# Kernel tuning notes

Hardware: AMD Instinct MI355X
Metric: run time of the kernel (lower is better)

## Reference

```python
import jax, jax.numpy as jnp
import numpy as np

IN_DIM, OUT_DIM = 128, 128
NUM, K = 5, 3            # knot intervals, spline order
SIZE = IN_DIM * OUT_DIM
BATCH = 512
NOISE = 0.1


def extend_knots_uniform(grid, k):
    # grid: (s, n_knots). Uniformly extend by k knots on each side.
    if k <= 0:
        return grid
    step = (grid[:, -1:] - grid[:, :1]) / (grid.shape[1] - 1)  # (s,1)
    left = grid[:, :1] - step * jnp.arange(k, 0, -1, dtype=grid.dtype)[None, :]
    right = grid[:, -1:] + step * jnp.arange(1, k + 1, dtype=grid.dtype)[None, :]
    return jnp.concatenate([left, grid, right], axis=1)


def cox_deboor(x, t, k):
    # x: (s, n), t: (s, m) extended knots -> B: (s, m-1-k, n)
    xt = x[:, None, :]                                   # (s,1,n)
    B = ((xt >= t[:, :-1, None]) & (xt < t[:, 1:, None])).astype(x.dtype)  # (s, m-1, n)
    m = t.shape[1]
    for r in range(1, k + 1):
        denom_a = jnp.maximum(t[:, r:m - 1] - t[:, :m - 1 - r], 1e-14)
        alpha = (xt - t[:, :m - 1 - r, None]) / denom_a[:, :, None]
        denom_b = jnp.maximum(t[:, r + 1:m] - t[:, 1:m - r], 1e-14)
        beta = (t[:, r + 1:m, None] - xt) / denom_b[:, :, None]
        B = alpha * B[:, :-1, :] + beta * B[:, 1:, :]    # (s, m-1-r, n)
    return B


def setup_inputs() -> dict:
    key = jax.random.key(0)
    kx, kc = jax.random.split(key)
    x = jax.random.normal(kx, (BATCH, IN_DIM), dtype=jnp.float32)
    knots = jnp.linspace(-1.0, 1.0, NUM + 1, dtype=jnp.float32)
    grid = jnp.tile(knots[None, :], (SIZE, 1))                       # (size, num+1)
    coef = jax.random.normal(kc, (SIZE, NUM + K), dtype=jnp.float32) * NOISE
    scale_base = jnp.ones((SIZE,), dtype=jnp.float32)
    scale_sp = jnp.ones((SIZE,), dtype=jnp.float32)
    mask = jnp.ones((SIZE,), dtype=jnp.float32)
    return {"x": x, "grid": grid, "coef": coef,
            "scale_base": scale_base, "scale_sp": scale_sp, "mask": mask}


def reference(x, grid, coef, scale_base, scale_sp, mask):
    batch = x.shape[0]
    # einsum('ij,k->ikj').reshape(b, size).T : row o*in_dim+i holds x[:, i]
    x_exp = jnp.tile(x, (1, OUT_DIM)).T                  # (size, batch)
    base_act = jax.nn.silu(x_exp)
    t_ext = extend_knots_uniform(grid, K)                # (size, num+1+2k)
    B = cox_deboor(x_exp, t_ext, K)                      # (size, num+k, batch)
    spline_val = jnp.einsum('sbn,sb->sn', B, coef)       # (size, batch)
    out = (scale_base[:, None] * base_act + scale_sp[:, None] * spline_val) * mask[:, None]
    out3 = out.reshape(OUT_DIM, IN_DIM, batch)           # permute(2,0,1).sum(dim=2)
    return out3.sum(axis=1).T                            # (batch, out_dim)
```

## Files before the change

kernel.cpp:

```cpp
#include <hip/hip_runtime.h>
#include <math.h>

constexpr int IN_DIM  = 128;
constexpr int OUT_DIM = 128;
constexpr int BATCH   = 512;
constexpr int NQ      = 8;
constexpr int TN = 8;
constexpr int TO = 32;
constexpr int NSEG = 8;
constexpr int SEGI = IN_DIM / NSEG;

__global__ __launch_bounds__(256, 1) void kan_kernel(
    const float* __restrict__ x,
    const float* __restrict__ grid,
    const float* __restrict__ coef,
    const float* __restrict__ scale_base,
    const float* __restrict__ scale_sp,
    const float* __restrict__ mask,
    float* __restrict__ out)
{
    __shared__ float Ps[TN][IN_DIM * NQ];
    __shared__ float Pb[TN][IN_DIM];
    __shared__ float red[NSEG][TN][TO];

    const int t  = threadIdx.x;
    const int n0 = (blockIdx.x >> 2) * TN;
    const int o0 = (blockIdx.x & 3) * TO;

    const float g0 = grid[0];
    const float g5 = grid[5];
    const float h  = (g5 - g0) * 0.2f;
    float tk[12];
    tk[0] = g0 - 3.f * h; tk[1] = g0 - 2.f * h; tk[2] = g0 - h;
    tk[3] = grid[0]; tk[4] = grid[1]; tk[5] = grid[2];
    tk[6] = grid[3]; tk[7] = grid[4]; tk[8] = grid[5];
    tk[9] = g5 + h; tk[10] = g5 + 2.f * h; tk[11] = g5 + 3.f * h;

    #pragma unroll
    for (int rep = 0; rep < 4; rep++) {
        const int p  = t + rep * 256;
        const int nl = p >> 7;
        const int i  = p & 127;
        const float xv = x[(n0 + nl) * IN_DIM + i];

        Pb[nl][i] = xv / (1.0f + __expf(-xv));

        float B[11];
        #pragma unroll
        for (int j = 0; j < 11; j++)
            B[j] = (xv >= tk[j] && xv < tk[j + 1]) ? 1.0f : 0.0f;
        #pragma unroll
        for (int r = 1; r <= 3; r++) {
            #pragma unroll
            for (int j = 0; j + r < 11; j++) {
                const float da = fmaxf(tk[j + r] - tk[j],     1e-14f);
                const float db = fmaxf(tk[j + r + 1] - tk[j + 1], 1e-14f);
                B[j] = (xv - tk[j]) / da * B[j] + (tk[j + r + 1] - xv) / db * B[j + 1];
            }
        }
        #pragma unroll
        for (int j = 0; j < NQ; j++) Ps[nl][i * NQ + j] = B[j];
    }
    __syncthreads();

    const int ol = t & 31;
    const int o  = o0 + ol;
    const int g  = t >> 5;

    float acc[TN];
    #pragma unroll
    for (int n = 0; n < TN; n++) acc[n] = 0.f;

    for (int ii = 0; ii < SEGI; ii++) {
        const int i = g * SEGI + ii;
        const int s = o * IN_DIM + i;
        const float4 c0 = ((const float4*)(coef + (size_t)s * NQ))[0];
        const float4 c1 = ((const float4*)(coef + (size_t)s * NQ))[1];
        const float m   = mask[s];
        const float vss = scale_sp[s]   * m;
        const float vsb = scale_base[s] * m;
        #pragma unroll
        for (int n = 0; n < TN; n++) {
            const float4* pr = (const float4*)(&Ps[n][i * NQ]);
            const float4 p0 = pr[0];
            const float4 p1 = pr[1];
            float d = p0.x * c0.x + p0.y * c0.y + p0.z * c0.z + p0.w * c0.w
                    + p1.x * c1.x + p1.y * c1.y + p1.z * c1.z + p1.w * c1.w;
            acc[n] += vss * d + vsb * Pb[n][i];
        }
    }

    #pragma unroll
    for (int n = 0; n < TN; n++) red[g][n][ol] = acc[n];
    __syncthreads();

    const int nl2 = t >> 5;
    float sum = 0.f;
    #pragma unroll
    for (int gg = 0; gg < NSEG; gg++) sum += red[gg][nl2][t & 31];
    out[(n0 + nl2) * OUT_DIM + (o0 + (t & 31))] = sum;
}

extern "C" void kernel_launch(void* const* d_in, const int* in_sizes, int n_in,
                              void* d_out, int out_size, void* d_ws, size_t ws_size,
                              hipStream_t stream) {
    const float* x          = (const float*)d_in[0];
    const float* grid       = (const float*)d_in[1];
    const float* coef       = (const float*)d_in[2];
    const float* scale_base = (const float*)d_in[3];
    const float* scale_sp   = (const float*)d_in[4];
    const float* mask       = (const float*)d_in[5];
    float* out = (float*)d_out;

    kan_kernel<<<dim3(256), dim3(256), 0, stream>>>(
        x, grid, coef, scale_base, scale_sp, mask, out);
}
```

Baseline: 80.73 us.

## Split input dimension across blocks with atomic accumulation and shared-memory coefficient staging

Each block now handles one 16-wide chunk of the input dimension for a 16-batch by 32-output tile, so the grid grows from 256 to 1024 blocks. Partial sums go to the output with atomicAdd after a memset. Coefficients are pre-scaled by scale_sp*mask and staged in XOR-swizzled shared memory so the inner loop reads only from LDS. B-spline work per thread drops to one element. In exchange there are eight atomic adds per output element, an extra memset launch, and a summation order that is no longer deterministic.

```diff
diff --git a/kernel.cpp b/kernel.cpp
--- a/kernel.cpp
+++ b/kernel.cpp
@@ -4,13 +4,11 @@
 constexpr int IN_DIM  = 128;
 constexpr int OUT_DIM = 128;
 constexpr int BATCH   = 512;
-constexpr int NQ      = 8;
-constexpr int TN = 8;
+constexpr int TN = 16;
 constexpr int TO = 32;
-constexpr int NSEG = 8;
-constexpr int SEGI = IN_DIM / NSEG;
+constexpr int IC = 16;
 
-__global__ __launch_bounds__(256, 1) void kan_kernel(
+__global__ __launch_bounds__(256, 4) void kan_main(
     const float* __restrict__ x,
     const float* __restrict__ grid,
     const float* __restrict__ coef,
@@ -19,13 +17,20 @@
     const float* __restrict__ mask,
     float* __restrict__ out)
 {
-    __shared__ float Ps[TN][IN_DIM * NQ];
-    __shared__ float Pb[TN][IN_DIM];
-    __shared__ float red[NSEG][TN][TO];
+    __shared__ float4 Cs0[TO * IC];
+    __shared__ float4 Cs1[TO * IC];
+    __shared__ float4 Ps4[TN * IC * 2];
+    __shared__ float  Vb[IC * TO];
+    __shared__ float  Pb[IC * TN];
 
     const int t  = threadIdx.x;
-    const int n0 = (blockIdx.x >> 2) * TN;
-    const int o0 = (blockIdx.x & 3) * TO;
+    const int b  = blockIdx.x;
+    const int ic = b & 7;
+    const int ot = (b >> 3) & 3;
+    const int nt = b >> 5;
+    const int i0 = ic * IC;
+    const int o0 = ot * TO;
+    const int n0 = nt * TN;
 
     const float g0 = grid[0];
     const float g5 = grid[5];
@@ -36,14 +41,10 @@
     tk[6] = grid[3]; tk[7] = grid[4]; tk[8] = grid[5];
     tk[9] = g5 + h; tk[10] = g5 + 2.f * h; tk[11] = g5 + 3.f * h;
 
-    #pragma unroll
-    for (int rep = 0; rep < 4; rep++) {
-        const int p  = t + rep * 256;
-        const int nl = p >> 7;
-        const int i  = p & 127;
-        const float xv = x[(n0 + nl) * IN_DIM + i];
-
-        Pb[nl][i] = xv / (1.0f + __expf(-xv));
+    {
+        const int nl = t >> 4;
+        const int il = t & 15;
+        const float xv = x[(n0 + nl) * IN_DIM + i0 + il];
 
         float B[11];
         #pragma unroll
@@ -53,52 +54,69 @@
         for (int r = 1; r <= 3; r++) {
             #pragma unroll
             for (int j = 0; j + r < 11; j++) {
-                const float da = fmaxf(tk[j + r] - tk[j],     1e-14f);
+                const float da = fmaxf(tk[j + r] - tk[j],         1e-14f);
                 const float db = fmaxf(tk[j + r + 1] - tk[j + 1], 1e-14f);
                 B[j] = (xv - tk[j]) / da * B[j] + (tk[j + r + 1] - xv) / db * B[j + 1];
             }
         }
-        #pragma unroll
-        for (int j = 0; j < NQ; j++) Ps[nl][i * NQ + j] = B[j];
+        Ps4[(nl * IC + il) * 2 + 0] = make_float4(B[0], B[1], B[2], B[3]);
+        Ps4[(nl * IC + il) * 2 + 1] = make_float4(B[4], B[5], B[6], B[7]);
+        Pb[il * TN + nl] = xv / (1.0f + __expf(-xv));
+    }
+
+    #pragma unroll
+    for (int r = 0; r < 4; r++) {
+        const int fi  = r * 256 + t;
+        const int o   = fi >> 5;
+        const int rem = fi & 31;
+        const int i   = rem >> 1;
+        const int hh  = rem & 1;
+        const int s   = (o0 + o) * IN_DIM + i0 + i;
+        float4 c = ((const float4*)coef)[(size_t)s * 2 + hh];
+        const float v = scale_sp[s] * mask[s];
+        c.x *= v; c.y *= v; c.z *= v; c.w *= v;
+        const int cidx = o * IC + (i ^ (o & 7));
+        if (hh) Cs1[cidx] = c; else Cs0[cidx] = c;
+    }
+    #pragma unroll
+    for (int r = 0; r < 2; r++) {
+        const int v = r * 256 + t;
+        const int o = v >> 4;
+        const int i = v & 15;
+        const int s = (o0 + o) * IN_DIM + i0 + i;
+        Vb[i * TO + o] = scale_base[s] * mask[s];
     }
     __syncthreads();
 
-    const int ol = t & 31;
-    const int o  = o0 + ol;
-    const int g  = t >> 5;
+    const int o  = t & 31;
+    const int nA = t >> 5;
+    const int nB = nA + 8;
+    const float4* __restrict__ psA = &Ps4[nA * IC * 2];
+    const float4* __restrict__ psB = &Ps4[nB * IC * 2];
+    const int osw = o & 7;
 
-    float acc[TN];
+    float accA = 0.f, accB = 0.f;
     #pragma unroll
-    for (int n = 0; n < TN; n++) acc[n] = 0.f;
-
-    for (int ii = 0; ii < SEGI; ii++) {
-        const int i = g * SEGI + ii;
-        const int s = o * IN_DIM + i;
-        const float4 c0 = ((const float4*)(coef + (size_t)s * NQ))[0];
-        const float4 c1 = ((const float4*)(coef + (size_t)s * NQ))[1];
-        const float m   = mask[s];
-        const float vss = scale_sp[s]   * m;
-        const float vsb = scale_base[s] * m;
-        #pragma unroll
-        for (int n = 0; n < TN; n++) {
-            const float4* pr = (const float4*)(&Ps[n][i * NQ]);
-            const float4 p0 = pr[0];
-            const float4 p1 = pr[1];
-            float d = p0.x * c0.x + p0.y * c0.y + p0.z * c0.z + p0.w * c0.w
-                    + p1.x * c1.x + p1.y * c1.y + p1.z * c1.z + p1.w * c1.w;
-            acc[n] += vss * d + vsb * Pb[n][i];
-        }
+    for (int i = 0; i < IC; i++) {
+        const int ci = o * IC + (i ^ osw);
+        const float4 c0 = Cs0[ci];
+        const float4 c1 = Cs1[ci];
+        const float4 a0 = psA[2 * i];
+        const float4 a1 = psA[2 * i + 1];
+        const float4 b0 = psB[2 * i];
+        const float4 b1 = psB[2 * i + 1];
+        const float vb  = Vb[i * TO + o];
+        const float pbA = Pb[i * TN + nA];
+        const float pbB = Pb[i * TN + nB];
+        accA += c0.x * a0.x + c0.y * a0.y + c0.z * a0.z + c0.w * a0.w
+              + c1.x * a1.x + c1.y * a1.y + c1.z * a1.z + c1.w * a1.w
+              + vb * pbA;
+        accB += c0.x * b0.x + c0.y * b0.y + c0.z * b0.z + c0.w * b0.w
+              + c1.x * b1.x + c1.y * b1.y + c1.z * b1.z + c1.w * b1.w
+              + vb * pbB;
     }
-
-    #pragma unroll
-    for (int n = 0; n < TN; n++) red[g][n][ol] = acc[n];
-    __syncthreads();
-
-    const int nl2 = t >> 5;
-    float sum = 0.f;
-    #pragma unroll
-    for (int gg = 0; gg < NSEG; gg++) sum += red[gg][nl2][t & 31];
-    out[(n0 + nl2) * OUT_DIM + (o0 + (t & 31))] = sum;
+    atomicAdd(&out[(n0 + nA) * OUT_DIM + o0 + o], accA);
+    atomicAdd(&out[(n0 + nB) * OUT_DIM + o0 + o], accB);
 }
 
 extern "C" void kernel_launch(void* const* d_in, const int* in_sizes, int n_in,
@@ -112,6 +130,8 @@
     const float* mask       = (const float*)d_in[5];
     float* out = (float*)d_out;
 
-    kan_kernel<<<dim3(256), dim3(256), 0, stream>>>(
+    hipMemsetAsync(out, 0, (size_t)out_size * sizeof(float), stream);
+
+    kan_main<<<dim3(1024), dim3(256), 0, stream>>>(
         x, grid, coef, scale_base, scale_sp, mask, out);
 }
```

Result: faster. 75.73 us (-6.2%).
